# Kernel tuning notes

Measured on AMD Instinct MI355X. Metric: run time of the kernel, lower is better.

## Reference

```python
import jax, jax.numpy as jnp
import numpy as np

C = 1.0          # curvature
SQC = 1.0        # sqrt(c)
MIN_NORM = 1e-15
PROJ_EPS = 4e-3  # float32 boundary eps (HGCN convention)

def _norm(x):
    return jnp.clip(jnp.linalg.norm(x, axis=-1, keepdims=True), MIN_NORM)

def logmap0(x):
    n = _norm(x)
    return jnp.arctanh(jnp.minimum(SQC * n, 1.0 - 1e-7)) * x / (SQC * n)

def expmap0(u):
    n = _norm(u)
    return jnp.tanh(SQC * n) * u / (SQC * n)

def proj(x):
    n = _norm(x)
    maxn = (1.0 - PROJ_EPS) / SQC
    return jnp.where(n > maxn, x / n * maxn, x)

def mobius_add(x, y):
    x2 = jnp.sum(x * x, -1, keepdims=True)
    y2 = jnp.sum(y * y, -1, keepdims=True)
    xy = jnp.sum(x * y, -1, keepdims=True)
    num = (1.0 + 2.0 * C * xy + C * y2) * x + (1.0 - C * x2) * y
    den = 1.0 + 2.0 * C * xy + C * C * x2 * y2
    return num / jnp.clip(den, MIN_NORM)

N, E, DIN, H, DH = 50000, 800000, 256, 4, 64  # heads*DH == out_features == 256

def setup_inputs() -> dict:
    key = jax.random.key(0)
    k1, k2, k3, k4, k5, k6, k7 = jax.random.split(key, 7)
    x = proj(0.01 * jax.random.normal(k1, (N, DIN), jnp.float32))  # points on the ball
    src = jax.random.randint(k2, (E,), 0, N)
    off = jax.random.randint(k3, (E,), 1, N)
    dst = (src + off) % N  # no self loops (remove_self_loops); added in reference
    edge_index = jnp.stack([src, dst]).astype(jnp.int64)
    glorot = float(np.sqrt(2.0 / (DIN + H * DH)))
    W = glorot * jax.random.normal(k4, (H * DH, DIN), jnp.float32)
    b_lin = 0.01 * jax.random.normal(k5, (H * DH,), jnp.float32)
    ga = float(np.sqrt(6.0 / (1 + 2 * DH)))
    att = jax.random.uniform(k6, (H, 2 * DH), jnp.float32, -ga, ga)
    b_conv = jnp.zeros((H * DH,), jnp.float32)
    return {"x": x, "edge_index": edge_index, "W": W, "b_lin": b_lin,
            "att": att, "b_conv": b_conv}

def reference(x, edge_index, W, b_lin, att, b_conv):
    n = x.shape[0]
    # HypLinear: mobius_matvec + hyperbolic bias (dropout=0, eval)
    xh = proj(expmap0(logmap0(x) @ W.T))
    hb = proj(expmap0(b_lin[None, :]))
    xh = proj(mobius_add(xh, hb))
    # add self loops (edge_index already has none)
    loop = jnp.arange(n)
    src = jnp.concatenate([edge_index[0], loop])
    dst = jnp.concatenate([edge_index[1], loop])
    # faithful to original: logmap0 then view(heads, -1, out_ch)
    logx = logmap0(xh).reshape(H, n, DH)  # [H,N,DH]
    # per-edge attention logits via per-node partial scores (same math as cat@att)
    s_i = jnp.einsum('hnd,hd->nh', logx, att[:, :DH])
    s_j = jnp.einsum('hnd,hd->nh', logx, att[:, DH:])
    alpha = jax.nn.leaky_relu(s_i[dst] + s_j[src], 0.2)  # [Etot,H]
    # segment softmax over incoming edges of each target node
    m = jax.ops.segment_max(alpha, dst, num_segments=n)
    a = jnp.exp(alpha - m[dst])
    ssum = jax.ops.segment_sum(a, dst, num_segments=n)
    a = a / jnp.clip(ssum[dst], MIN_NORM)
    # gather source messages, weight, scatter-add
    xj = jnp.take(logx, src, axis=1).transpose(1, 0, 2)  # [Etot,H,DH]
    out = jax.ops.segment_sum(xj * a[:, :, None], dst, num_segments=n)  # [N,H,DH]
    # faithful to original update(): [H,N,DH].view(-1, H*DH) + bias
    out = out.transpose(1, 0, 2).reshape(n, H * DH) + b_conv
    out = jax.nn.relu(out)  # act between proj_tan0 (identity for Poincare)
    return proj(expmap0(out))
```

## Files before the change

kernel.cpp:

```cpp
#include <hip/hip_runtime.h>

#define MIN_NORM 1e-15f
#define MAXN (1.0f - 4e-3f)

typedef __attribute__((ext_vector_type(8))) short short8;
typedef __attribute__((ext_vector_type(4))) float f32x4;

__device__ __forceinline__ float bf2f(unsigned short u) {
  union { unsigned int i; float f; } c; c.i = ((unsigned int)u) << 16; return c.f;
}
__device__ __forceinline__ unsigned short f2bf(float f) {
  union { float f; unsigned int i; } c; c.f = f;
  unsigned int r = c.i + 0x7FFFu + ((c.i >> 16) & 1u);
  return (unsigned short)(r >> 16);
}
__device__ __forceinline__ float wave_sum(float v) {
#pragma unroll
  for (int off = 32; off > 0; off >>= 1) v += __shfl_xor(v, off, 64);
  return v;
}
__device__ __forceinline__ float gsum16(float v) {
#pragma unroll
  for (int off = 8; off > 0; off >>= 1) v += __shfl_xor(v, off, 64);
  return v;
}
__device__ __forceinline__ float tanh_fast(float x) {
  float e = __expf(2.0f * x);
  return (e - 1.0f) / (e + 1.0f);
}
__device__ __forceinline__ float atanh_fast(float x) {
  return 0.5f * __logf((1.0f + x) / (1.0f - x));
}

__global__ __launch_bounds__(256) void k_prep(const float* __restrict__ x,
                                              const float* __restrict__ W,
                                              const float* __restrict__ b_lin,
                                              float* __restrict__ rs,
                                              unsigned short* __restrict__ xb,
                                              unsigned short* __restrict__ Wb,
                                              float* __restrict__ hb,
                                              float* __restrict__ hb2,
                                              int* __restrict__ cnt,
                                              unsigned short* __restrict__ slots, int N) {
  int row = blockIdx.x * 4 + (threadIdx.x >> 6);
  int lane = threadIdx.x & 63;
  float4 u = *(const float4*)(x + (size_t)row * 256 + lane * 4);
  ushort4 st;
  st.x = f2bf(u.x); st.y = f2bf(u.y); st.z = f2bf(u.z); st.w = f2bf(u.w);
  *(ushort4*)(xb + (size_t)row * 256 + lane * 4) = st;
  float s = wave_sum(u.x * u.x + u.y * u.y + u.z * u.z + u.w * u.w);
  if (lane == 0) {
    float n = fmaxf(sqrtf(s), MIN_NORM);
    rs[row] = atanhf(fminf(n, 1.0f - 1e-7f)) / n;
  }
  int g = blockIdx.x * 256 + threadIdx.x;
  if (g < N) { cnt[g] = 1; slots[(size_t)g * 64] = (unsigned short)g; }
  if (blockIdx.x < 32) {
    int g2 = blockIdx.x * 256 + threadIdx.x;
    int ln = g2 & 63, fj = g2 >> 6;
    int kk = fj >> 4, hf = (fj >> 3) & 1, j = fj & 7;
    int lc2 = ln & 15, qd2 = ln >> 4;
    const float* src = W + (size_t)(((hf * 8 + j) * 16 + lc2) * 256 + kk * 32 + qd2 * 8);
    float4 a = *(const float4*)src;
    float4 b = *(const float4*)(src + 4);
    unsigned short* dst = Wb + (size_t)g2 * 8;
    dst[0] = f2bf(a.x); dst[1] = f2bf(a.y); dst[2] = f2bf(a.z); dst[3] = f2bf(a.w);
    dst[4] = f2bf(b.x); dst[5] = f2bf(b.y); dst[6] = f2bf(b.z); dst[7] = f2bf(b.w);
  }
  if (blockIdx.x == 64 && threadIdx.x < 64) {
    float4 b4 = ((const float4*)b_lin)[lane];
    float bx = b4.x, by = b4.y, bz = b4.z, bw = b4.w;
    float sb = wave_sum(bx * bx + by * by + bz * bz + bw * bw);
    float n1 = fmaxf(sqrtf(sb), MIN_NORM);
    float t = tanhf(n1) / n1;
    bx *= t; by *= t; bz *= t; bw *= t;
    float s2 = wave_sum(bx * bx + by * by + bz * bz + bw * bw);
    float n2 = fmaxf(sqrtf(s2), MIN_NORM);
    if (n2 > MAXN) { float f = MAXN / n2; bx *= f; by *= f; bz *= f; bw *= f; }
    float4 o; o.x = bx; o.y = by; o.z = bz; o.w = bw;
    ((float4*)hb)[lane] = o;
    float s3 = wave_sum(bx * bx + by * by + bz * bz + bw * bw);
    if (lane == 0) *hb2 = s3;
  }
}

__global__ __launch_bounds__(256) void k_gemmfill(const unsigned short* __restrict__ xb,
                                                  const unsigned short* __restrict__ Wb,
                                                  const float* __restrict__ rs,
                                                  const float* __restrict__ hb,
                                                  const float* __restrict__ hb2p,
                                                  const float* __restrict__ att,
                                                  unsigned short* __restrict__ L,
                                                  float* __restrict__ s_i,
                                                  float* __restrict__ s_j,
                                                  const int* __restrict__ ei,
                                                  int* __restrict__ cnt,
                                                  unsigned short* __restrict__ slots,
                                                  int E, int M, int NQ) {
  int r5 = blockIdx.x % 5, q5 = blockIdx.x / 5;
  if (r5 != 0) {
    int fid = q5 * 4 + (r5 - 1);
    int e = fid * 256 + (int)threadIdx.x;
    if (e < E) {
      int s = ei[e];
      int d = ei[E + e];
      int pos = atomicAdd(&cnt[d], 1);
      if (pos < 64) slots[(size_t)d * 64 + pos] = (unsigned short)s;
    }
    return;
  }
  int tid = threadIdx.x;
  int wv = tid >> 6, lane = tid & 63, qd = lane >> 4, lc = lane & 15;
  int i0 = q5 * 64;
  int arow = i0 + wv * 16 + lc;
  if (arow >= M) arow = M - 1;
  short8 af[8];
#pragma unroll
  for (int kk = 0; kk < 8; ++kk)
    af[kk] = *(const short8*)(xb + (size_t)arow * 256 + kk * 32 + qd * 8);
  f32x4 acc[16];
#pragma unroll
  for (int jt = 0; jt < 16; ++jt) acc[jt] = (f32x4){0.f, 0.f, 0.f, 0.f};
#pragma unroll
  for (int kk = 0; kk < 8; ++kk) {
#pragma unroll
    for (int half = 0; half < 2; ++half) {
      short8 bf[8];
#pragma unroll
      for (int j = 0; j < 8; ++j)
        bf[j] = *(const short8*)(Wb + (size_t)(((kk * 2 + half) * 8 + j) * 64 + lane) * 8);
#pragma unroll
      for (int j = 0; j < 8; ++j)
        acc[half * 8 + j] =
            __builtin_amdgcn_mfma_f32_16x16x32_bf16(af[kk], bf[j], acc[half * 8 + j], 0, 0, 0);
    }
  }
  float y2 = *hb2p;
  float hbreg[16];
#pragma unroll
  for (int jt = 0; jt < 16; ++jt) hbreg[jt] = hb[jt * 16 + lc];

#pragma unroll
  for (int r = 0; r < 4; ++r) {
    int row_r = i0 + wv * 16 + qd * 4 + r;
    bool valid = row_r < M;
    int rr = valid ? row_r : M - 1;
    float rsv = rs[rr];
    float v[16];
    float ss = 0.0f, xyr = 0.0f;
#pragma unroll
    for (int jt = 0; jt < 16; ++jt) {
      v[jt] = rsv * acc[jt][r];
      ss += v[jt] * v[jt];
      xyr += v[jt] * hbreg[jt];
    }
    ss = gsum16(ss);
    xyr = gsum16(xyr);
    float n1 = fmaxf(sqrtf(ss), MIN_NORM);
    float e1 = tanh_fast(n1) / n1;
    float n2 = e1 * n1;
    float f2 = (n2 > MAXN) ? MAXN / n2 : 1.0f;
    float e12 = e1 * f2;
    float nx = n2 * f2;
    float x2 = nx * nx;
#pragma unroll
    for (int jt = 0; jt < 16; ++jt) v[jt] *= e12;
    float xy = e12 * xyr;
    float c1 = 1.0f + 2.0f * xy + y2;
    float c2 = 1.0f - x2;
    float den = fmaxf(1.0f + 2.0f * xy + x2 * y2, MIN_NORM);
    float inv = 1.0f / den;
    float s3 = inv * inv * (c1 * c1 * x2 + 2.0f * c1 * c2 * xy + c2 * c2 * y2);
    float n3 = fmaxf(sqrtf(s3), MIN_NORM);
    float f3 = (n3 > MAXN) ? MAXN / n3 : 1.0f;
    float n4 = fmaxf(n3 * f3, MIN_NORM);
    float sc = atanh_fast(n4) / n4;
    float g = inv * f3 * sc;
    float Lv[16];
#pragma unroll
    for (int jt = 0; jt < 16; ++jt) Lv[jt] = (c1 * v[jt] + c2 * hbreg[jt]) * g;
    int h_r = row_r / NQ;
    int q_r = row_r - h_r * NQ;
    if (valid) {
#pragma unroll
      for (int jt = 0; jt < 16; ++jt) {
        int n = q_r * 4 + (jt >> 2);
        int d = (jt & 3) * 16 + lc;
        L[(size_t)n * 256 + h_r * 64 + d] = f2bf(Lv[jt]);
      }
    }
    float pig[4], pjg[4];
#pragma unroll
    for (int g4 = 0; g4 < 4; ++g4) {
      float pi = 0.0f, pj = 0.0f;
#pragma unroll
      for (int t = 0; t < 4; ++t) {
        float a_i = att[h_r * 128 + t * 16 + lc];
        float a_j = att[h_r * 128 + 64 + t * 16 + lc];
        pi += Lv[g4 * 4 + t] * a_i;
        pj += Lv[g4 * 4 + t] * a_j;
      }
      pig[g4] = gsum16(pi);
      pjg[g4] = gsum16(pj);
    }
    if (valid && lc == 0) {
#pragma unroll
      for (int g4 = 0; g4 < 4; ++g4) {
        int n = q_r * 4 + g4;
        s_i[n * 4 + h_r] = pig[g4];
        s_j[n * 4 + h_r] = pjg[g4];
      }
    }
  }
}

__global__ __launch_bounds__(256) void HGATLayer_49246095016355_kernel(
    const unsigned short* __restrict__ L,
    const float* __restrict__ s_i,
    const float* __restrict__ s_j,
    const int* __restrict__ cnt,
    const unsigned short* __restrict__ slots,
    const float* __restrict__ b_conv,
    float* __restrict__ out, int N, int NQ) {
  int q = blockIdx.x;
  int w = threadIdx.x >> 6, lane = threadIdx.x & 63;
  int n = q * 4 + w;
  int deg = min(cnt[n], 64);
  float4 si4 = *(const float4*)(s_i + n * 4);
  int src_l = n;
  float4 a4 = {-1e30f, -1e30f, -1e30f, -1e30f};
  if (lane < deg) {
    src_l = slots[(size_t)n * 64 + lane];
    float4 sj4 = *(const float4*)(s_j + src_l * 4);
    float t0 = si4.x + sj4.x, t1 = si4.y + sj4.y, t2 = si4.z + sj4.z, t3 = si4.w + sj4.w;
    a4.x = (t0 > 0.f) ? t0 : 0.2f * t0;
    a4.y = (t1 > 0.f) ? t1 : 0.2f * t1;
    a4.z = (t2 > 0.f) ? t2 : 0.2f * t2;
    a4.w = (t3 > 0.f) ? t3 : 0.2f * t3;
  }
  float4 mx = a4;
#pragma unroll
  for (int off = 32; off > 0; off >>= 1) {
    mx.x = fmaxf(mx.x, __shfl_xor(mx.x, off, 64));
    mx.y = fmaxf(mx.y, __shfl_xor(mx.y, off, 64));
    mx.z = fmaxf(mx.z, __shfl_xor(mx.z, off, 64));
    mx.w = fmaxf(mx.w, __shfl_xor(mx.w, off, 64));
  }
  float4 p4 = {0.f, 0.f, 0.f, 0.f};
  if (lane < deg) {
    p4.x = __expf(a4.x - mx.x); p4.y = __expf(a4.y - mx.y);
    p4.z = __expf(a4.z - mx.z); p4.w = __expf(a4.w - mx.w);
  }
  float4 sm = p4;
#pragma unroll
  for (int off = 32; off > 0; off >>= 1) {
    sm.x += __shfl_xor(sm.x, off, 64);
    sm.y += __shfl_xor(sm.y, off, 64);
    sm.z += __shfl_xor(sm.z, off, 64);
    sm.w += __shfl_xor(sm.w, off, 64);
  }
  __shared__ int   s_src[4][64];
  __shared__ float s_w[4][64][4];
  s_src[w][lane] = src_l;
  *(float4*)&s_w[w][lane][0] = p4;

  int c = lane & 31, ep = lane >> 5, hc = c >> 3;
  float smh = (hc == 0) ? sm.x : (hc == 1) ? sm.y : (hc == 2) ? sm.z : sm.w;

  float accv[8];
#pragma unroll
  for (int j = 0; j < 8; ++j) accv[j] = 0.f;
  int np2 = (deg + 1) >> 1;
  int nb = (np2 + 7) >> 3;
  for (int b = 0; b < nb; ++b) {
    int kbase = b * 16 + ep;
    int ks[8];
#pragma unroll
    for (int p = 0; p < 8; ++p) ks[p] = s_src[w][kbase + 2 * p];
    short8 r[8];
#pragma unroll
    for (int p = 0; p < 8; ++p)
      r[p] = *(const short8*)(L + (size_t)ks[p] * 256 + c * 8);
    float wk[8];
#pragma unroll
    for (int p = 0; p < 8; ++p) wk[p] = s_w[w][kbase + 2 * p][hc];
#pragma unroll
    for (int p = 0; p < 8; ++p) {
#pragma unroll
      for (int j = 0; j < 8; ++j)
        accv[j] = fmaf(wk[p], bf2f((unsigned short)r[p][j]), accv[j]);
    }
  }
#pragma unroll
  for (int j = 0; j < 8; ++j) accv[j] += __shfl_xor(accv[j], 32, 64);

  float isum = 1.0f / fmaxf(smh, MIN_NORM);
  const float* bcp = b_conv + w * 64 + (c & 7) * 8;
  float vv[8];
  float ps = 0.f;
#pragma unroll
  for (int j = 0; j < 8; ++j) {
    float t = fmaxf(accv[j] * isum + bcp[j], 0.0f);
    vv[j] = t;
    ps += t * t;
  }
#pragma unroll
  for (int off = 1; off < 8; off <<= 1) ps += __shfl_xor(ps, off, 64);
  __shared__ float red[4][4];
  if (lane < 32 && (c & 7) == 0) red[w][hc] = ps;
  __syncthreads();
  float tot = red[0][hc] + red[1][hc] + red[2][hc] + red[3][hc];
  float nraw = sqrtf(tot);
  float ncl = fmaxf(nraw, MIN_NORM);
  float t = tanhf(ncl) / ncl;
  float ny = fmaxf(t * nraw, MIN_NORM);
  float f = (ny > MAXN) ? (MAXN / ny) : 1.0f;
  float tf = t * f;
  if (lane < 32) {
    float4 y0; y0.x = tf * vv[0]; y0.y = tf * vv[1]; y0.z = tf * vv[2]; y0.w = tf * vv[3];
    float4 y1; y1.x = tf * vv[4]; y1.y = tf * vv[5]; y1.z = tf * vv[6]; y1.w = tf * vv[7];
    float* op = out + (size_t)(hc * NQ + q) * 256 + w * 64 + (c & 7) * 8;
    *(float4*)op = y0;
    *(float4*)(op + 4) = y1;
  }
}

extern "C" void kernel_launch(void* const* d_in, const int* in_sizes, int n_in,
                              void* d_out, int out_size, void* d_ws, size_t ws_size,
                              hipStream_t stream) {
  const float* x   = (const float*)d_in[0];
  const int*   ei  = (const int*)d_in[1];
  const float* W   = (const float*)d_in[2];
  const float* bl  = (const float*)d_in[3];
  const float* att = (const float*)d_in[4];
  const float* bc  = (const float*)d_in[5];
  float* out = (float*)d_out;

  const int N = in_sizes[0] / 256;
  const int E = in_sizes[1] / 2;
  const int NQ = N / 4;

  unsigned short* xb = (unsigned short*)d_out;

  char* w = (char*)d_ws;
  unsigned short* L  = (unsigned short*)w; w += (size_t)N * 256 * 2;
  unsigned short* Wb = (unsigned short*)w; w += 65536 * 2;
  float* s_i = (float*)w; w += (size_t)N * 4 * 4;
  float* s_j = (float*)w; w += (size_t)N * 4 * 4;
  float* rs  = (float*)w; w += (size_t)N * 4;
  float* hb  = (float*)w; w += 256 * 4;
  float* hb2 = (float*)w; w += 16;
  int* cnt   = (int*)w;   w += (size_t)N * 4;
  unsigned short* slots = (unsigned short*)w;

  const int GB = (N + 63) / 64;
  k_prep<<<N / 4, 256, 0, stream>>>(x, W, bl, rs, xb, Wb, hb, hb2, cnt, slots, N);
  k_gemmfill<<<GB * 5, 256, 0, stream>>>(xb, Wb, rs, hb, hb2, att, L, s_i, s_j,
                                         ei, cnt, slots, E, N, NQ);
  HGATLayer_49246095016355_kernel<<<NQ, 256, 0, stream>>>(L, s_i, s_j, cnt, slots, bc, out, N, NQ);
}
```

Before: 255.6 us.

## Split aggregation kernel per head and cap edge loop at two fixed batches

The aggregation kernel now launches one block per (node quad, head) instead of one block per node quad handling all four heads. Each wave computes the softmax for a single head and gathers only that head's 64-column slice of L, with 8 edge groups of 8 lanes over at most 64 edges in two unrolled batches. The goal is more parallelism and less per-thread work, in exchange for recomputing slot and score loads four times and issuing smaller gathers. It also switches tanhf to tanh_fast.

New measurement: 277.3 us. 8.5% more time.

```diff
diff --git a/kernel.cpp b/kernel.cpp
--- a/kernel.cpp
+++ b/kernel.cpp
@@ -222,104 +222,101 @@
     const unsigned short* __restrict__ slots,
     const float* __restrict__ b_conv,
     float* __restrict__ out, int N, int NQ) {
-  int q = blockIdx.x;
+  int hc = blockIdx.x & 3;
+  int q = blockIdx.x >> 2;
   int w = threadIdx.x >> 6, lane = threadIdx.x & 63;
   int n = q * 4 + w;
   int deg = min(cnt[n], 64);
-  float4 si4 = *(const float4*)(s_i + n * 4);
+  float si = s_i[n * 4 + hc];
   int src_l = n;
-  float4 a4 = {-1e30f, -1e30f, -1e30f, -1e30f};
+  float a = -1e30f;
   if (lane < deg) {
     src_l = slots[(size_t)n * 64 + lane];
-    float4 sj4 = *(const float4*)(s_j + src_l * 4);
-    float t0 = si4.x + sj4.x, t1 = si4.y + sj4.y, t2 = si4.z + sj4.z, t3 = si4.w + sj4.w;
-    a4.x = (t0 > 0.f) ? t0 : 0.2f * t0;
-    a4.y = (t1 > 0.f) ? t1 : 0.2f * t1;
-    a4.z = (t2 > 0.f) ? t2 : 0.2f * t2;
-    a4.w = (t3 > 0.f) ? t3 : 0.2f * t3;
-  }
-  float4 mx = a4;
-#pragma unroll
-  for (int off = 32; off > 0; off >>= 1) {
-    mx.x = fmaxf(mx.x, __shfl_xor(mx.x, off, 64));
-    mx.y = fmaxf(mx.y, __shfl_xor(mx.y, off, 64));
-    mx.z = fmaxf(mx.z, __shfl_xor(mx.z, off, 64));
-    mx.w = fmaxf(mx.w, __shfl_xor(mx.w, off, 64));
-  }
-  float4 p4 = {0.f, 0.f, 0.f, 0.f};
-  if (lane < deg) {
-    p4.x = __expf(a4.x - mx.x); p4.y = __expf(a4.y - mx.y);
-    p4.z = __expf(a4.z - mx.z); p4.w = __expf(a4.w - mx.w);
-  }
-  float4 sm = p4;
-#pragma unroll
-  for (int off = 32; off > 0; off >>= 1) {
-    sm.x += __shfl_xor(sm.x, off, 64);
-    sm.y += __shfl_xor(sm.y, off, 64);
-    sm.z += __shfl_xor(sm.z, off, 64);
-    sm.w += __shfl_xor(sm.w, off, 64);
-  }
+    float t0 = si + s_j[src_l * 4 + hc];
+    a = (t0 > 0.f) ? t0 : 0.2f * t0;
+  }
+  float mx = a;
+#pragma unroll
+  for (int off = 32; off > 0; off >>= 1) mx = fmaxf(mx, __shfl_xor(mx, off, 64));
+  float p = (lane < deg) ? __expf(a - mx) : 0.f;
+  float sm = p;
+#pragma unroll
+  for (int off = 32; off > 0; off >>= 1) sm += __shfl_xor(sm, off, 64);
+
   __shared__ int   s_src[4][64];
-  __shared__ float s_w[4][64][4];
+  __shared__ float s_p[4][64];
   s_src[w][lane] = src_l;
-  *(float4*)&s_w[w][lane][0] = p4;
-
-  int c = lane & 31, ep = lane >> 5, hc = c >> 3;
-  float smh = (hc == 0) ? sm.x : (hc == 1) ? sm.y : (hc == 2) ? sm.z : sm.w;
-
+  s_p[w][lane] = p;
+
+  int g = lane >> 3, j = lane & 7;
   float accv[8];
 #pragma unroll
-  for (int j = 0; j < 8; ++j) accv[j] = 0.f;
-  int np2 = (deg + 1) >> 1;
-  int nb = (np2 + 7) >> 3;
-  for (int b = 0; b < nb; ++b) {
-    int kbase = b * 16 + ep;
-    int ks[8];
-#pragma unroll
-    for (int p = 0; p < 8; ++p) ks[p] = s_src[w][kbase + 2 * p];
-    short8 r[8];
-#pragma unroll
-    for (int p = 0; p < 8; ++p)
-      r[p] = *(const short8*)(L + (size_t)ks[p] * 256 + c * 8);
-    float wk[8];
-#pragma unroll
-    for (int p = 0; p < 8; ++p) wk[p] = s_w[w][kbase + 2 * p][hc];
-#pragma unroll
-    for (int p = 0; p < 8; ++p) {
-#pragma unroll
-      for (int j = 0; j < 8; ++j)
-        accv[j] = fmaf(wk[p], bf2f((unsigned short)r[p][j]), accv[j]);
-    }
-  }
-#pragma unroll
-  for (int j = 0; j < 8; ++j) accv[j] += __shfl_xor(accv[j], 32, 64);
-
-  float isum = 1.0f / fmaxf(smh, MIN_NORM);
-  const float* bcp = b_conv + w * 64 + (c & 7) * 8;
+  for (int i = 0; i < 8; ++i) accv[i] = 0.f;
+  {
+    short8 r[4];
+    float wk[4];
+#pragma unroll
+    for (int t = 0; t < 4; ++t) {
+      int k = t * 8 + g;
+      int s = s_src[w][k];
+      r[t] = *(const short8*)(L + (size_t)s * 256 + hc * 64 + j * 8);
+      wk[t] = s_p[w][k];
+    }
+#pragma unroll
+    for (int t = 0; t < 4; ++t)
+#pragma unroll
+      for (int i = 0; i < 8; ++i)
+        accv[i] = fmaf(wk[t], bf2f((unsigned short)r[t][i]), accv[i]);
+    if (deg > 32) {
+#pragma unroll
+      for (int t = 0; t < 4; ++t) {
+        int k = 32 + t * 8 + g;
+        int s = s_src[w][k];
+        r[t] = *(const short8*)(L + (size_t)s * 256 + hc * 64 + j * 8);
+        wk[t] = s_p[w][k];
+      }
+#pragma unroll
+      for (int t = 0; t < 4; ++t)
+#pragma unroll
+        for (int i = 0; i < 8; ++i)
+          accv[i] = fmaf(wk[t], bf2f((unsigned short)r[t][i]), accv[i]);
+    }
+  }
+#pragma unroll
+  for (int i = 0; i < 8; ++i) {
+    accv[i] += __shfl_xor(accv[i], 8, 64);
+    accv[i] += __shfl_xor(accv[i], 16, 64);
+    accv[i] += __shfl_xor(accv[i], 32, 64);
+  }
+  float isum = 1.0f / fmaxf(sm, MIN_NORM);
+  float4 b0 = *(const float4*)(b_conv + w * 64 + j * 8);
+  float4 b1 = *(const float4*)(b_conv + w * 64 + j * 8 + 4);
+  float bc[8] = {b0.x, b0.y, b0.z, b0.w, b1.x, b1.y, b1.z, b1.w};
   float vv[8];
   float ps = 0.f;
 #pragma unroll
-  for (int j = 0; j < 8; ++j) {
-    float t = fmaxf(accv[j] * isum + bcp[j], 0.0f);
-    vv[j] = t;
+  for (int i = 0; i < 8; ++i) {
+    float t = fmaxf(accv[i] * isum + bc[i], 0.f);
+    vv[i] = t;
     ps += t * t;
   }
-#pragma unroll
-  for (int off = 1; off < 8; off <<= 1) ps += __shfl_xor(ps, off, 64);
-  __shared__ float red[4][4];
-  if (lane < 32 && (c & 7) == 0) red[w][hc] = ps;
+  ps += __shfl_xor(ps, 1, 64);
+  ps += __shfl_xor(ps, 2, 64);
+  ps += __shfl_xor(ps, 4, 64);
+  __shared__ float red[4];
+  if (lane == 0) red[w] = ps;
   __syncthreads();
-  float tot = red[0][hc] + red[1][hc] + red[2][hc] + red[3][hc];
+  float tot = red[0] + red[1] + red[2] + red[3];
   float nraw = sqrtf(tot);
   float ncl = fmaxf(nraw, MIN_NORM);
-  float t = tanhf(ncl) / ncl;
+  float t = tanh_fast(ncl) / ncl;
   float ny = fmaxf(t * nraw, MIN_NORM);
   float f = (ny > MAXN) ? (MAXN / ny) : 1.0f;
   float tf = t * f;
-  if (lane < 32) {
+  if (g == 0) {
     float4 y0; y0.x = tf * vv[0]; y0.y = tf * vv[1]; y0.z = tf * vv[2]; y0.w = tf * vv[3];
     float4 y1; y1.x = tf * vv[4]; y1.y = tf * vv[5]; y1.z = tf * vv[6]; y1.w = tf * vv[7];
-    float* op = out + (size_t)(hc * NQ + q) * 256 + w * 64 + (c & 7) * 8;
+    float* op = out + (size_t)(hc * NQ + q) * 256 + w * 64 + j * 8;
     *(float4*)op = y0;
     *(float4*)(op + 4) = y1;
   }
@@ -357,5 +354,5 @@
   k_prep<<<N / 4, 256, 0, stream>>>(x, W, bl, rs, xb, Wb, hb, hb2, cnt, slots, N);
   k_gemmfill<<<GB * 5, 256, 0, stream>>>(xb, Wb, rs, hb, hb2, att, L, s_i, s_j,
                                          ei, cnt, slots, E, N, NQ);
-  HGATLayer_49246095016355_kernel<<<NQ, 256, 0, stream>>>(L, s_i, s_j, cnt, slots, bc, out, N, NQ);
-}
+  HGATLayer_49246095016355_kernel<<<NQ * 4, 256, 0, stream>>>(L, s_i, s_j, cnt, slots, bc, out, N, NQ);
+}
```
